# Kernel tuning notes

Hardware: AMD Instinct MI355X
Metric: run time of the kernel (lower is better)

The kernel has to match this reference:

```python
import jax, jax.numpy as jnp
import numpy as np

N_NODES = 50000
N_EDGES = 1600000
IN_F = 128
HEADS = 4
HEAD_DIM = 32  # out_features // heads = 128 // 4
NEG_SLOPE = 0.2


def setup_inputs() -> dict:
    key = jax.random.key(0)
    k1, k2, k3, k4 = jax.random.split(key, 4)
    x = jax.random.normal(k1, (N_NODES, IN_F), dtype=jnp.float32)
    edge_index = jax.random.randint(k2, (2, N_EDGES), 0, N_NODES, dtype=jnp.int64)
    # xavier-uniform-ish scaling for params
    W = jax.random.normal(k3, (HEADS * HEAD_DIM, IN_F), dtype=jnp.float32) * (1.0 / np.sqrt(IN_F))
    a = jax.random.normal(k4, (HEADS, 2 * HEAD_DIM), dtype=jnp.float32) * (1.0 / np.sqrt(2 * HEAD_DIM))
    return {"x": x, "edge_index": edge_index, "W": W, "a": a}


def reference(x, edge_index, W, a):
    # x: [N, F_in], edge_index: [2, E], W: [H*D, F_in], a: [H, 2D]
    N = x.shape[0]
    h = (x @ W.T).reshape(N, HEADS, HEAD_DIM)  # [N, H, D]
    src, dst = edge_index[0], edge_index[1]
    a_src = a[:, :HEAD_DIM]  # [H, D]
    a_dst = a[:, HEAD_DIM:]  # [H, D]
    h_src = h[src]  # [E, H, D]
    h_dst = h[dst]  # [E, H, D]
    # equivalent to (cat([h_src, h_dst], -1) * a).sum(-1), without materializing edge_h
    att = jnp.einsum('ehd,hd->eh', h_src, a_src) + jnp.einsum('ehd,hd->eh', h_dst, a_dst)
    att = jax.nn.leaky_relu(att, negative_slope=NEG_SLOPE)  # [E, H]
    msgs = att[..., None] * h_src  # [E, H, D]
    out = jax.ops.segment_sum(msgs, dst, num_segments=N)  # [N, H, D]
    # dropout is identity in eval/deterministic reference
    return out.reshape(N, HEADS * HEAD_DIM)
```

## Files before the change

kernel.cpp:

```cpp
#include <hip/hip_runtime.h>

#define N_NODES 50000
#define N_EDGES 1600000
#define IN_F 128
#define OUT_F 128
#define HEADS 4
#define HEAD_DIM 32
#define NEG_SLOPE 0.2f

#define NB 391
#define CAP 4800
#define P1_EPT 16
#define P1_EPB (P1_EPT * 256)
#define GEMM_BLOCKS ((N_NODES + 63) / 64)
#define PART_BLOCKS ((N_EDGES + P1_EPB - 1) / P1_EPB)

typedef __attribute__((ext_vector_type(8))) short short8v;
typedef __attribute__((ext_vector_type(4))) float f32x4;

__device__ __forceinline__ unsigned short f2bf(float f) {
    unsigned u = __builtin_bit_cast(unsigned, f);
    u += 0x7FFFu + ((u >> 16) & 1u);
    return (unsigned short)(u >> 16);
}
__device__ __forceinline__ float bf_lo(unsigned v) {
    return __builtin_bit_cast(float, v << 16);
}
__device__ __forceinline__ float bf_hi(unsigned v) {
    return __builtin_bit_cast(float, v & 0xFFFF0000u);
}

__global__ __launch_bounds__(256) void prep_kernel(
    const float* __restrict__ W, unsigned short* __restrict__ wbf,
    int* __restrict__ gcursor)
{
    int t = blockIdx.x * 256 + threadIdx.x;
    if (t < 16384) wbf[t] = f2bf(W[t]);
    if (t < NB) gcursor[t] = t * CAP;
}

__global__ __launch_bounds__(256) void fused_gp_kernel(
    const float* __restrict__ x, const unsigned short* __restrict__ wbf,
    const float* __restrict__ a,
    unsigned short* __restrict__ hb,
    float* __restrict__ alpha_s, float* __restrict__ alpha_d,
    const int* __restrict__ ei, int* __restrict__ gcursor,
    unsigned* __restrict__ part)
{
    __shared__ int cnt[NB];
    __shared__ int gbase[NB];

    const int tid = threadIdx.x;

    if (blockIdx.x < GEMM_BLOCKS) {
        const int wave = tid >> 6;
        const int lane = tid & 63;
        const int lr = lane & 15;
        const int lg = lane >> 4;
        const int nodeA = blockIdx.x * 64 + wave * 16 + lr;
        const int nrow = nodeA < N_NODES ? nodeA : 0;

        f32x4 acc[8];
        #pragma unroll
        for (int i = 0; i < 8; ++i) acc[i] = (f32x4){0.f, 0.f, 0.f, 0.f};

        #pragma unroll
        for (int ks = 0; ks < 4; ++ks) {
            const float* xp = x + (size_t)nrow * 128 + ks * 32 + lg * 8;
            float4 xa = *(const float4*)xp;
            float4 xc = *(const float4*)(xp + 4);
            short8v afrag;
            afrag[0] = (short)f2bf(xa.x); afrag[1] = (short)f2bf(xa.y);
            afrag[2] = (short)f2bf(xa.z); afrag[3] = (short)f2bf(xa.w);
            afrag[4] = (short)f2bf(xc.x); afrag[5] = (short)f2bf(xc.y);
            afrag[6] = (short)f2bf(xc.z); afrag[7] = (short)f2bf(xc.w);
            #pragma unroll
            for (int nf = 0; nf < 8; ++nf) {
                const short8v bfrag = *(const short8v*)(wbf + (size_t)(nf * 16 + lr) * 128 + ks * 32 + lg * 8);
                acc[nf] = __builtin_amdgcn_mfma_f32_16x16x32_bf16(afrag, bfrag, acc[nf], 0, 0, 0);
            }
        }

        float as_c[8], ad_c[8];
        #pragma unroll
        for (int nf = 0; nf < 8; ++nf) {
            const int idx = (nf >> 1) * 64 + (nf & 1) * 16 + lr;
            as_c[nf] = a[idx];
            ad_c[nf] = a[idx + 32];
        }

        const int nbase = blockIdx.x * 64 + wave * 16 + lg * 4;
        #pragma unroll
        for (int reg = 0; reg < 4; ++reg) {
            const int n2 = nbase + reg;
            if (n2 < N_NODES) {
                unsigned short* hp = hb + (size_t)n2 * 128 + lr;
                #pragma unroll
                for (int nf = 0; nf < 8; ++nf)
                    hp[nf * 16] = f2bf(acc[nf][reg]);
            }
            float sh[4], th[4];
            #pragma unroll
            for (int hd = 0; hd < 4; ++hd) {
                sh[hd] = acc[2 * hd][reg] * as_c[2 * hd] + acc[2 * hd + 1][reg] * as_c[2 * hd + 1];
                th[hd] = acc[2 * hd][reg] * ad_c[2 * hd] + acc[2 * hd + 1][reg] * ad_c[2 * hd + 1];
            }
            #pragma unroll
            for (int off = 8; off >= 1; off >>= 1) {
                #pragma unroll
                for (int hd = 0; hd < 4; ++hd) {
                    sh[hd] += __shfl_xor(sh[hd], off);
                    th[hd] += __shfl_xor(th[hd], off);
                }
            }
            if (lr == 0 && n2 < N_NODES) {
                #pragma unroll
                for (int hd = 0; hd < 4; ++hd) {
                    alpha_s[n2 * 4 + hd] = sh[hd];
                    alpha_d[n2 * 4 + hd] = th[hd];
                }
            }
        }
    } else {
        const int e0 = (blockIdx.x - GEMM_BLOCKS) * P1_EPB;

        for (int i = tid; i < NB; i += 256) cnt[i] = 0;
        __syncthreads();

        unsigned pk[P1_EPT];
        int bk[P1_EPT];
        int loc[P1_EPT];
        #pragma unroll
        for (int c4 = 0; c4 < P1_EPT / 4; ++c4) {
            int e = e0 + c4 * 1024 + tid * 4;
            if (e < N_EDGES) {
                int4 s4 = *(const int4*)(ei + e);
                int4 d4 = *(const int4*)(ei + N_EDGES + e);
                int ss[4] = {s4.x, s4.y, s4.z, s4.w};
                int dd[4] = {d4.x, d4.y, d4.z, d4.w};
                #pragma unroll
                for (int j = 0; j < 4; ++j) {
                    int k = c4 * 4 + j;
                    int bb = dd[j] >> 7;
                    bk[k] = bb;
                    pk[k] = ((unsigned)(dd[j] & 127) << 16) | (unsigned)ss[j];
                    loc[k] = atomicAdd(&cnt[bb], 1);
                }
            } else {
                #pragma unroll
                for (int j = 0; j < 4; ++j) bk[c4 * 4 + j] = -1;
            }
        }
        __syncthreads();
        for (int bq = tid; bq < NB; bq += 256)
            gbase[bq] = atomicAdd(&gcursor[bq], cnt[bq]);
        __syncthreads();
        #pragma unroll
        for (int k = 0; k < P1_EPT; ++k)
            if (bk[k] >= 0)
                part[gbase[bk[k]] + loc[k]] = pk[k];
    }
}

__global__ __launch_bounds__(256) void bucket_kernel(
    const int* __restrict__ gcursor, const unsigned* __restrict__ part,
    unsigned short* __restrict__ srcs16,
    int* __restrict__ node_start, int* __restrict__ node_cnt)
{
    __shared__ unsigned ent[CAP];
    __shared__ unsigned short srt[CAP];
    __shared__ int cnt4[4][128];
    __shared__ int sc[128];
    __shared__ int cur4[4][128];

    const int b = blockIdx.x;
    const int tid = threadIdx.x;
    const int w = tid >> 6;
    const int bstart = b * CAP;
    int n_b = gcursor[b] - bstart;
    if (n_b > CAP) n_b = CAP;

    if (tid < 128) {
        cnt4[0][tid] = 0; cnt4[1][tid] = 0; cnt4[2][tid] = 0; cnt4[3][tid] = 0;
    }
    __syncthreads();

    for (int i = tid; i < n_b; i += 256) {
        unsigned e = part[bstart + i];
        ent[i] = e;
        atomicAdd(&cnt4[w][e >> 16], 1);
    }
    __syncthreads();

    int c = 0;
    if (tid < 128) {
        c = cnt4[0][tid] + cnt4[1][tid] + cnt4[2][tid] + cnt4[3][tid];
        sc[tid] = c;
    }
    __syncthreads();
    #pragma unroll
    for (int off = 1; off < 128; off <<= 1) {
        int v = 0;
        if (tid < 128 && tid >= off) v = sc[tid - off];
        __syncthreads();
        if (tid < 128) sc[tid] += v;
        __syncthreads();
    }
    if (tid < 128) {
        int eb = sc[tid] - c;
        int c0 = cnt4[0][tid], c1 = cnt4[1][tid], c2 = cnt4[2][tid];
        cur4[0][tid] = eb;
        cur4[1][tid] = eb + c0;
        cur4[2][tid] = eb + c0 + c1;
        cur4[3][tid] = eb + c0 + c1 + c2;
        const int node = b * 128 + tid;
        if (node < N_NODES) {
            node_start[node] = bstart + eb;
            node_cnt[node] = c;
        }
    }
    __syncthreads();

    for (int i = tid; i < n_b; i += 256) {
        unsigned e = ent[i];
        int loc = atomicAdd(&cur4[w][e >> 16], 1);
        srt[loc] = (unsigned short)(e & 0xFFFFu);
    }
    __syncthreads();

    const unsigned* srt32 = (const unsigned*)srt;
    unsigned* dst32 = (unsigned*)(srcs16 + bstart);
    const int nw2 = (n_b + 1) >> 1;
    for (int i = tid; i < nw2; i += 256) dst32[i] = srt32[i];
}

__global__ __launch_bounds__(256) void gather_kernel(
    const unsigned short* __restrict__ srcs,
    const int* __restrict__ node_start, const int* __restrict__ node_cnt,
    const unsigned* __restrict__ h32,
    const float* __restrict__ alpha_s, const float* __restrict__ alpha_d,
    float* __restrict__ out)
{
    const int wid = (blockIdx.x * 256 + threadIdx.x) >> 6;
    if (wid >= N_NODES) return;
    const int lane = threadIdx.x & 63;
    const int start = node_start[wid];
    const int end = start + node_cnt[wid];
    const int head = lane >> 4;

    const float adv = alpha_d[wid * 4 + head];

    float a0x = 0.f, a0y = 0.f, a1x = 0.f, a1y = 0.f;
    float a2x = 0.f, a2y = 0.f, a3x = 0.f, a3y = 0.f;
    int i = start;
    for (; i + 7 < end; i += 8) {
        int s0 = srcs[i],     s1 = srcs[i + 1], s2 = srcs[i + 2], s3 = srcs[i + 3];
        int s4 = srcs[i + 4], s5 = srcs[i + 5], s6 = srcs[i + 6], s7 = srcs[i + 7];
        float t0 = alpha_s[s0 * 4 + head] + adv;
        float t1 = alpha_s[s1 * 4 + head] + adv;
        float t2 = alpha_s[s2 * 4 + head] + adv;
        float t3 = alpha_s[s3 * 4 + head] + adv;
        float t4 = alpha_s[s4 * 4 + head] + adv;
        float t5 = alpha_s[s5 * 4 + head] + adv;
        float t6 = alpha_s[s6 * 4 + head] + adv;
        float t7 = alpha_s[s7 * 4 + head] + adv;
        t0 = t0 > 0.f ? t0 : NEG_SLOPE * t0;
        t1 = t1 > 0.f ? t1 : NEG_SLOPE * t1;
        t2 = t2 > 0.f ? t2 : NEG_SLOPE * t2;
        t3 = t3 > 0.f ? t3 : NEG_SLOPE * t3;
        t4 = t4 > 0.f ? t4 : NEG_SLOPE * t4;
        t5 = t5 > 0.f ? t5 : NEG_SLOPE * t5;
        t6 = t6 > 0.f ? t6 : NEG_SLOPE * t6;
        t7 = t7 > 0.f ? t7 : NEG_SLOPE * t7;
        unsigned v0 = h32[(size_t)s0 * 64 + lane];
        unsigned v1 = h32[(size_t)s1 * 64 + lane];
        unsigned v2 = h32[(size_t)s2 * 64 + lane];
        unsigned v3 = h32[(size_t)s3 * 64 + lane];
        unsigned v4 = h32[(size_t)s4 * 64 + lane];
        unsigned v5 = h32[(size_t)s5 * 64 + lane];
        unsigned v6 = h32[(size_t)s6 * 64 + lane];
        unsigned v7 = h32[(size_t)s7 * 64 + lane];
        a0x = fmaf(t0, bf_lo(v0), a0x); a0y = fmaf(t0, bf_hi(v0), a0y);
        a1x = fmaf(t1, bf_lo(v1), a1x); a1y = fmaf(t1, bf_hi(v1), a1y);
        a2x = fmaf(t2, bf_lo(v2), a2x); a2y = fmaf(t2, bf_hi(v2), a2y);
        a3x = fmaf(t3, bf_lo(v3), a3x); a3y = fmaf(t3, bf_hi(v3), a3y);
        a0x = fmaf(t4, bf_lo(v4), a0x); a0y = fmaf(t4, bf_hi(v4), a0y);
        a1x = fmaf(t5, bf_lo(v5), a1x); a1y = fmaf(t5, bf_hi(v5), a1y);
        a2x = fmaf(t6, bf_lo(v6), a2x); a2y = fmaf(t6, bf_hi(v6), a2y);
        a3x = fmaf(t7, bf_lo(v7), a3x); a3y = fmaf(t7, bf_hi(v7), a3y);
    }
    for (; i + 1 < end; i += 2) {
        int s0 = srcs[i], s1 = srcs[i + 1];
        float t0 = alpha_s[s0 * 4 + head] + adv;
        float t1 = alpha_s[s1 * 4 + head] + adv;
        t0 = t0 > 0.f ? t0 : NEG_SLOPE * t0;
        t1 = t1 > 0.f ? t1 : NEG_SLOPE * t1;
        unsigned v0 = h32[(size_t)s0 * 64 + lane];
        unsigned v1 = h32[(size_t)s1 * 64 + lane];
        a0x = fmaf(t0, bf_lo(v0), a0x); a0y = fmaf(t0, bf_hi(v0), a0y);
        a1x = fmaf(t1, bf_lo(v1), a1x); a1y = fmaf(t1, bf_hi(v1), a1y);
    }
    if (i < end) {
        int s0 = srcs[i];
        float t0 = alpha_s[s0 * 4 + head] + adv;
        t0 = t0 > 0.f ? t0 : NEG_SLOPE * t0;
        unsigned v0 = h32[(size_t)s0 * 64 + lane];
        a2x = fmaf(t0, bf_lo(v0), a2x); a2y = fmaf(t0, bf_hi(v0), a2y);
    }
    float2 r = {(a0x + a1x) + (a2x + a3x), (a0y + a1y) + (a2y + a3y)};
    ((float2*)out)[(size_t)wid * 64 + lane] = r;
}

__global__ __launch_bounds__(256) void edge_kernel(
    const int* __restrict__ ei,
    const unsigned* __restrict__ h32,
    const float* __restrict__ alpha_s, const float* __restrict__ alpha_d,
    float* __restrict__ out)
{
    const unsigned total = (unsigned)N_EDGES * 32u;
    const unsigned stride = gridDim.x * blockDim.x;
    for (unsigned i = blockIdx.x * blockDim.x + threadIdx.x; i < total; i += stride) {
        const int e = (int)(i >> 5);
        const int c = (int)(i & 31);
        const int src = ei[e];
        const int dst = ei[N_EDGES + e];
        const int head = c >> 3;

        float att = alpha_s[src * 4 + head] + alpha_d[dst * 4 + head];
        att = att > 0.f ? att : NEG_SLOPE * att;

        unsigned v0 = h32[(size_t)src * 64 + c * 2];
        unsigned v1 = h32[(size_t)src * 64 + c * 2 + 1];
        float* po = out + (size_t)dst * 128 + c * 4;
        atomicAdd(po + 0, att * bf_lo(v0));
        atomicAdd(po + 1, att * bf_hi(v0));
        atomicAdd(po + 2, att * bf_lo(v1));
        atomicAdd(po + 3, att * bf_hi(v1));
    }
}

extern "C" void kernel_launch(void* const* d_in, const int* in_sizes, int n_in,
                              void* d_out, int out_size, void* d_ws, size_t ws_size,
                              hipStream_t stream) {
    const float* x  = (const float*)d_in[0];
    const int*   ei = (const int*)d_in[1];
    const float* W  = (const float*)d_in[2];
    const float* a  = (const float*)d_in[3];
    float* out = (float*)d_out;

    unsigned short* hb = (unsigned short*)d_ws;
    float* as = (float*)(hb + (size_t)N_NODES * 128);
    float* ad = as + (size_t)N_NODES * 4;
    unsigned* part = (unsigned*)(ad + (size_t)N_NODES * 4);
    unsigned short* srcs16 = (unsigned short*)(part + (size_t)NB * CAP);
    int* gcursor = (int*)(srcs16 + (size_t)NB * CAP);
    int* node_start = gcursor + 512;
    int* node_cnt   = node_start + 50176;
    unsigned short* wbf = (unsigned short*)(node_cnt + 50176);
    const size_t needed = (size_t)((char*)(wbf + 16384) - (char*)d_ws);

    prep_kernel<<<64, 256, 0, stream>>>(W, wbf, gcursor);

    if (ws_size >= needed) {
        fused_gp_kernel<<<GEMM_BLOCKS + PART_BLOCKS, 256, 0, stream>>>(
            x, wbf, a, hb, as, ad, ei, gcursor, part);
        bucket_kernel<<<NB, 256, 0, stream>>>(gcursor, part, srcs16, node_start, node_cnt);
        gather_kernel<<<(N_NODES * 64 + 255) / 256, 256, 0, stream>>>(
            srcs16, node_start, node_cnt, (const unsigned*)hb, as, ad, out);
    } else {
        fused_gp_kernel<<<GEMM_BLOCKS, 256, 0, stream>>>(
            x, wbf, a, hb, as, ad, ei, gcursor, part);
        hipMemsetAsync(d_out, 0, (size_t)out_size * sizeof(float), stream);
        edge_kernel<<<4096, 256, 0, stream>>>(ei, (const unsigned*)hb, as, ad, out);
    }
}
```

Before: 106.3 us.

## Fuse bucket sort and per-node gather into one 1024-thread kernel

Merges the bucket-sorting kernel and the gather kernel, so each block sorts its 128-node bucket in LDS and then its 16 waves process 8 nodes each, reading source indices directly from shared memory. This removes the global write and reread of the sorted index array and the node start/count arrays, and saves one kernel launch. In exchange only 391 blocks do the gather, which may limit occupancy and latency hiding for the random h loads, and load imbalance across nodes within a wave's serial loop may grow.

```diff
diff --git a/kernel.cpp b/kernel.cpp
--- a/kernel.cpp
+++ b/kernel.cpp
@@ -162,39 +162,41 @@
     }
 }
 
-__global__ __launch_bounds__(256) void bucket_kernel(
+__global__ __launch_bounds__(1024) void bucket_gather_kernel(
     const int* __restrict__ gcursor, const unsigned* __restrict__ part,
-    unsigned short* __restrict__ srcs16,
-    int* __restrict__ node_start, int* __restrict__ node_cnt)
+    const unsigned* __restrict__ h32,
+    const float* __restrict__ alpha_s, const float* __restrict__ alpha_d,
+    float* __restrict__ out)
 {
     __shared__ unsigned ent[CAP];
     __shared__ unsigned short srt[CAP];
-    __shared__ int cnt4[4][128];
+    __shared__ int cnt8[8][128];
     __shared__ int sc[128];
-    __shared__ int cur4[4][128];
+    __shared__ int cur8[8][128];
+    __shared__ int nstart[128];
+    __shared__ int ncnt[128];
 
     const int b = blockIdx.x;
     const int tid = threadIdx.x;
-    const int w = tid >> 6;
+    const int sg = tid >> 7;
     const int bstart = b * CAP;
     int n_b = gcursor[b] - bstart;
     if (n_b > CAP) n_b = CAP;
 
-    if (tid < 128) {
-        cnt4[0][tid] = 0; cnt4[1][tid] = 0; cnt4[2][tid] = 0; cnt4[3][tid] = 0;
-    }
-    __syncthreads();
-
-    for (int i = tid; i < n_b; i += 256) {
+    for (int i = tid; i < 8 * 128; i += 1024) (&cnt8[0][0])[i] = 0;
+    __syncthreads();
+
+    for (int i = tid; i < n_b; i += 1024) {
         unsigned e = part[bstart + i];
         ent[i] = e;
-        atomicAdd(&cnt4[w][e >> 16], 1);
+        atomicAdd(&cnt8[sg][e >> 16], 1);
     }
     __syncthreads();
 
     int c = 0;
     if (tid < 128) {
-        c = cnt4[0][tid] + cnt4[1][tid] + cnt4[2][tid] + cnt4[3][tid];
+        #pragma unroll
+        for (int s = 0; s < 8; ++s) c += cnt8[s][tid];
         sc[tid] = c;
     }
     __syncthreads();
@@ -208,107 +210,93 @@
     }
     if (tid < 128) {
         int eb = sc[tid] - c;
-        int c0 = cnt4[0][tid], c1 = cnt4[1][tid], c2 = cnt4[2][tid];
-        cur4[0][tid] = eb;
-        cur4[1][tid] = eb + c0;
-        cur4[2][tid] = eb + c0 + c1;
-        cur4[3][tid] = eb + c0 + c1 + c2;
-        const int node = b * 128 + tid;
-        if (node < N_NODES) {
-            node_start[node] = bstart + eb;
-            node_cnt[node] = c;
-        }
-    }
-    __syncthreads();
-
-    for (int i = tid; i < n_b; i += 256) {
+        nstart[tid] = eb;
+        ncnt[tid] = c;
+        int run = eb;
+        #pragma unroll
+        for (int s = 0; s < 8; ++s) { cur8[s][tid] = run; run += cnt8[s][tid]; }
+    }
+    __syncthreads();
+
+    for (int i = tid; i < n_b; i += 1024) {
         unsigned e = ent[i];
-        int loc = atomicAdd(&cur4[w][e >> 16], 1);
+        int loc = atomicAdd(&cur8[sg][e >> 16], 1);
         srt[loc] = (unsigned short)(e & 0xFFFFu);
     }
     __syncthreads();
 
-    const unsigned* srt32 = (const unsigned*)srt;
-    unsigned* dst32 = (unsigned*)(srcs16 + bstart);
-    const int nw2 = (n_b + 1) >> 1;
-    for (int i = tid; i < nw2; i += 256) dst32[i] = srt32[i];
-}
-
-__global__ __launch_bounds__(256) void gather_kernel(
-    const unsigned short* __restrict__ srcs,
-    const int* __restrict__ node_start, const int* __restrict__ node_cnt,
-    const unsigned* __restrict__ h32,
-    const float* __restrict__ alpha_s, const float* __restrict__ alpha_d,
-    float* __restrict__ out)
-{
-    const int wid = (blockIdx.x * 256 + threadIdx.x) >> 6;
-    if (wid >= N_NODES) return;
-    const int lane = threadIdx.x & 63;
-    const int start = node_start[wid];
-    const int end = start + node_cnt[wid];
+    const int wave = tid >> 6;
+    const int lane = tid & 63;
     const int head = lane >> 4;
 
-    const float adv = alpha_d[wid * 4 + head];
-
-    float a0x = 0.f, a0y = 0.f, a1x = 0.f, a1y = 0.f;
-    float a2x = 0.f, a2y = 0.f, a3x = 0.f, a3y = 0.f;
-    int i = start;
-    for (; i + 7 < end; i += 8) {
-        int s0 = srcs[i],     s1 = srcs[i + 1], s2 = srcs[i + 2], s3 = srcs[i + 3];
-        int s4 = srcs[i + 4], s5 = srcs[i + 5], s6 = srcs[i + 6], s7 = srcs[i + 7];
-        float t0 = alpha_s[s0 * 4 + head] + adv;
-        float t1 = alpha_s[s1 * 4 + head] + adv;
-        float t2 = alpha_s[s2 * 4 + head] + adv;
-        float t3 = alpha_s[s3 * 4 + head] + adv;
-        float t4 = alpha_s[s4 * 4 + head] + adv;
-        float t5 = alpha_s[s5 * 4 + head] + adv;
-        float t6 = alpha_s[s6 * 4 + head] + adv;
-        float t7 = alpha_s[s7 * 4 + head] + adv;
-        t0 = t0 > 0.f ? t0 : NEG_SLOPE * t0;
-        t1 = t1 > 0.f ? t1 : NEG_SLOPE * t1;
-        t2 = t2 > 0.f ? t2 : NEG_SLOPE * t2;
-        t3 = t3 > 0.f ? t3 : NEG_SLOPE * t3;
-        t4 = t4 > 0.f ? t4 : NEG_SLOPE * t4;
-        t5 = t5 > 0.f ? t5 : NEG_SLOPE * t5;
-        t6 = t6 > 0.f ? t6 : NEG_SLOPE * t6;
-        t7 = t7 > 0.f ? t7 : NEG_SLOPE * t7;
-        unsigned v0 = h32[(size_t)s0 * 64 + lane];
-        unsigned v1 = h32[(size_t)s1 * 64 + lane];
-        unsigned v2 = h32[(size_t)s2 * 64 + lane];
-        unsigned v3 = h32[(size_t)s3 * 64 + lane];
-        unsigned v4 = h32[(size_t)s4 * 64 + lane];
-        unsigned v5 = h32[(size_t)s5 * 64 + lane];
-        unsigned v6 = h32[(size_t)s6 * 64 + lane];
-        unsigned v7 = h32[(size_t)s7 * 64 + lane];
-        a0x = fmaf(t0, bf_lo(v0), a0x); a0y = fmaf(t0, bf_hi(v0), a0y);
-        a1x = fmaf(t1, bf_lo(v1), a1x); a1y = fmaf(t1, bf_hi(v1), a1y);
-        a2x = fmaf(t2, bf_lo(v2), a2x); a2y = fmaf(t2, bf_hi(v2), a2y);
-        a3x = fmaf(t3, bf_lo(v3), a3x); a3y = fmaf(t3, bf_hi(v3), a3y);
-        a0x = fmaf(t4, bf_lo(v4), a0x); a0y = fmaf(t4, bf_hi(v4), a0y);
-        a1x = fmaf(t5, bf_lo(v5), a1x); a1y = fmaf(t5, bf_hi(v5), a1y);
-        a2x = fmaf(t6, bf_lo(v6), a2x); a2y = fmaf(t6, bf_hi(v6), a2y);
-        a3x = fmaf(t7, bf_lo(v7), a3x); a3y = fmaf(t7, bf_hi(v7), a3y);
-    }
-    for (; i + 1 < end; i += 2) {
-        int s0 = srcs[i], s1 = srcs[i + 1];
-        float t0 = alpha_s[s0 * 4 + head] + adv;
-        float t1 = alpha_s[s1 * 4 + head] + adv;
-        t0 = t0 > 0.f ? t0 : NEG_SLOPE * t0;
-        t1 = t1 > 0.f ? t1 : NEG_SLOPE * t1;
-        unsigned v0 = h32[(size_t)s0 * 64 + lane];
-        unsigned v1 = h32[(size_t)s1 * 64 + lane];
-        a0x = fmaf(t0, bf_lo(v0), a0x); a0y = fmaf(t0, bf_hi(v0), a0y);
-        a1x = fmaf(t1, bf_lo(v1), a1x); a1y = fmaf(t1, bf_hi(v1), a1y);
-    }
-    if (i < end) {
-        int s0 = srcs[i];
-        float t0 = alpha_s[s0 * 4 + head] + adv;
-        t0 = t0 > 0.f ? t0 : NEG_SLOPE * t0;
-        unsigned v0 = h32[(size_t)s0 * 64 + lane];
-        a2x = fmaf(t0, bf_lo(v0), a2x); a2y = fmaf(t0, bf_hi(v0), a2y);
-    }
-    float2 r = {(a0x + a1x) + (a2x + a3x), (a0y + a1y) + (a2y + a3y)};
-    ((float2*)out)[(size_t)wid * 64 + lane] = r;
+    for (int k = 0; k < 8; ++k) {
+        const int ln = wave * 8 + k;
+        const int n = b * 128 + ln;
+        if (n >= N_NODES) break;
+        const int start = nstart[ln];
+        const int end = start + ncnt[ln];
+        const float adv = alpha_d[n * 4 + head];
+
+        float a0x = 0.f, a0y = 0.f, a1x = 0.f, a1y = 0.f;
+        float a2x = 0.f, a2y = 0.f, a3x = 0.f, a3y = 0.f;
+        int i = start;
+        for (; i + 7 < end; i += 8) {
+            int s0 = srt[i],     s1 = srt[i + 1], s2 = srt[i + 2], s3 = srt[i + 3];
+            int s4 = srt[i + 4], s5 = srt[i + 5], s6 = srt[i + 6], s7 = srt[i + 7];
+            float t0 = alpha_s[s0 * 4 + head] + adv;
+            float t1 = alpha_s[s1 * 4 + head] + adv;
+            float t2 = alpha_s[s2 * 4 + head] + adv;
+            float t3 = alpha_s[s3 * 4 + head] + adv;
+            float t4 = alpha_s[s4 * 4 + head] + adv;
+            float t5 = alpha_s[s5 * 4 + head] + adv;
+            float t6 = alpha_s[s6 * 4 + head] + adv;
+            float t7 = alpha_s[s7 * 4 + head] + adv;
+            t0 = t0 > 0.f ? t0 : NEG_SLOPE * t0;
+            t1 = t1 > 0.f ? t1 : NEG_SLOPE * t1;
+            t2 = t2 > 0.f ? t2 : NEG_SLOPE * t2;
+            t3 = t3 > 0.f ? t3 : NEG_SLOPE * t3;
+            t4 = t4 > 0.f ? t4 : NEG_SLOPE * t4;
+            t5 = t5 > 0.f ? t5 : NEG_SLOPE * t5;
+            t6 = t6 > 0.f ? t6 : NEG_SLOPE * t6;
+            t7 = t7 > 0.f ? t7 : NEG_SLOPE * t7;
+            unsigned v0 = h32[(size_t)s0 * 64 + lane];
+            unsigned v1 = h32[(size_t)s1 * 64 + lane];
+            unsigned v2 = h32[(size_t)s2 * 64 + lane];
+            unsigned v3 = h32[(size_t)s3 * 64 + lane];
+            unsigned v4 = h32[(size_t)s4 * 64 + lane];
+            unsigned v5 = h32[(size_t)s5 * 64 + lane];
+            unsigned v6 = h32[(size_t)s6 * 64 + lane];
+            unsigned v7 = h32[(size_t)s7 * 64 + lane];
+            a0x = fmaf(t0, bf_lo(v0), a0x); a0y = fmaf(t0, bf_hi(v0), a0y);
+            a1x = fmaf(t1, bf_lo(v1), a1x); a1y = fmaf(t1, bf_hi(v1), a1y);
+            a2x = fmaf(t2, bf_lo(v2), a2x); a2y = fmaf(t2, bf_hi(v2), a2y);
+            a3x = fmaf(t3, bf_lo(v3), a3x); a3y = fmaf(t3, bf_hi(v3), a3y);
+            a0x = fmaf(t4, bf_lo(v4), a0x); a0y = fmaf(t4, bf_hi(v4), a0y);
+            a1x = fmaf(t5, bf_lo(v5), a1x); a1y = fmaf(t5, bf_hi(v5), a1y);
+            a2x = fmaf(t6, bf_lo(v6), a2x); a2y = fmaf(t6, bf_hi(v6), a2y);
+            a3x = fmaf(t7, bf_lo(v7), a3x); a3y = fmaf(t7, bf_hi(v7), a3y);
+        }
+        for (; i + 1 < end; i += 2) {
+            int s0 = srt[i], s1 = srt[i + 1];
+            float t0 = alpha_s[s0 * 4 + head] + adv;
+            float t1 = alpha_s[s1 * 4 + head] + adv;
+            t0 = t0 > 0.f ? t0 : NEG_SLOPE * t0;
+            t1 = t1 > 0.f ? t1 : NEG_SLOPE * t1;
+            unsigned v0 = h32[(size_t)s0 * 64 + lane];
+            unsigned v1 = h32[(size_t)s1 * 64 + lane];
+            a0x = fmaf(t0, bf_lo(v0), a0x); a0y = fmaf(t0, bf_hi(v0), a0y);
+            a1x = fmaf(t1, bf_lo(v1), a1x); a1y = fmaf(t1, bf_hi(v1), a1y);
+        }
+        if (i < end) {
+            int s0 = srt[i];
+            float t0 = alpha_s[s0 * 4 + head] + adv;
+            t0 = t0 > 0.f ? t0 : NEG_SLOPE * t0;
+            unsigned v0 = h32[(size_t)s0 * 64 + lane];
+            a2x = fmaf(t0, bf_lo(v0), a2x); a2y = fmaf(t0, bf_hi(v0), a2y);
+        }
+        float2 r = {(a0x + a1x) + (a2x + a3x), (a0y + a1y) + (a2y + a3y)};
+        ((float2*)out)[(size_t)n * 64 + lane] = r;
+    }
 }
 
 __global__ __launch_bounds__(256) void edge_kernel(
@@ -352,11 +340,8 @@
     float* as = (float*)(hb + (size_t)N_NODES * 128);
     float* ad = as + (size_t)N_NODES * 4;
     unsigned* part = (unsigned*)(ad + (size_t)N_NODES * 4);
-    unsigned short* srcs16 = (unsigned short*)(part + (size_t)NB * CAP);
-    int* gcursor = (int*)(srcs16 + (size_t)NB * CAP);
-    int* node_start = gcursor + 512;
-    int* node_cnt   = node_start + 50176;
-    unsigned short* wbf = (unsigned short*)(node_cnt + 50176);
+    int* gcursor = (int*)(part + (size_t)NB * CAP);
+    unsigned short* wbf = (unsigned short*)(gcursor + 512);
     const size_t needed = (size_t)((char*)(wbf + 16384) - (char*)d_ws);
 
     prep_kernel<<<64, 256, 0, stream>>>(W, wbf, gcursor);
@@ -364,9 +349,8 @@
     if (ws_size >= needed) {
         fused_gp_kernel<<<GEMM_BLOCKS + PART_BLOCKS, 256, 0, stream>>>(
             x, wbf, a, hb, as, ad, ei, gcursor, part);
-        bucket_kernel<<<NB, 256, 0, stream>>>(gcursor, part, srcs16, node_start, node_cnt);
-        gather_kernel<<<(N_NODES * 64 + 255) / 256, 256, 0, stream>>>(
-            srcs16, node_start, node_cnt, (const unsigned*)hb, as, ad, out);
+        bucket_gather_kernel<<<NB, 1024, 0, stream>>>(
+            gcursor, part, (const unsigned*)hb, as, ad, out);
     } else {
         fused_gp_kernel<<<GEMM_BLOCKS, 256, 0, stream>>>(
             x, wbf, a, hb, as, ad, ei, gcursor, part);
```

After: 108.9 us. +2.4%, slower.
